# Optimization experiments

Hardware: AMD Instinct MI355X
Metric: run time of the kernel (lower is better)

## Reference

```python
import jax, jax.numpy as jnp
import numpy as np

N, E, D, H, G, C = 50000, 800000, 3, 128, 64, 10

def setup_inputs() -> dict:
    key = jax.random.key(0)
    ks = jax.random.split(key, 10)
    s = 0.1  # small init scale
    return {
        "pos": jax.random.normal(ks[0], (N, D), jnp.float32),
        "edge_index": jax.random.randint(ks[1], (2, E), 0, N, dtype=jnp.int64),
        "batch": jnp.sort(jax.random.randint(ks[2], (N,), 0, G, dtype=jnp.int64)),
        "W1": jax.random.normal(ks[3], (D, H), jnp.float32) * s,
        "b1": jnp.zeros((H,), jnp.float32),
        "W2": jax.random.normal(ks[4], (H, H), jnp.float32) * s,
        "b2": jnp.zeros((H,), jnp.float32),
        "W3": jax.random.normal(ks[5], (H, H), jnp.float32) * s,
        "b3": jnp.zeros((H,), jnp.float32),
        "Wl1": jax.random.normal(ks[6], (H, H // 2), jnp.float32) * s,
        "bl1": jnp.zeros((H // 2,), jnp.float32),
        "Wl2": jax.random.normal(ks[7], (H // 2, C), jnp.float32) * s,
        "bl2": jnp.zeros((C,), jnp.float32),
        "num_graphs": G,
    }

def reference(pos, edge_index, batch, W1, b1, W2, b2, W3, b3, Wl1, bl1, Wl2, bl2, num_graphs):
    n = pos.shape[0]
    loop = jnp.arange(n, dtype=edge_index.dtype)
    # GCN: add self-loops, symmetric normalization deg^-1/2 (A+I) deg^-1/2
    src = jnp.concatenate([edge_index[0], loop])
    dst = jnp.concatenate([edge_index[1], loop])
    deg = jax.ops.segment_sum(jnp.ones(src.shape, pos.dtype), dst, num_segments=n)
    dinv = jax.lax.rsqrt(jnp.maximum(deg, 1e-12))  # deg >= 1 due to self-loops
    norm = dinv[src] * dinv[dst]  # [E+N]

    def gcn(x, W, b):
        h = x @ W                               # [N,F] dense transform first (PyG order)
        msg = h[src] * norm[:, None]            # gather + normalize
        return jax.ops.segment_sum(msg, dst, num_segments=n) + b  # scatter-add

    x = jax.nn.relu(gcn(pos, W1, b1))   # dropout = identity (eval mode)
    x = jax.nn.relu(gcn(x, W2, b2))
    x = jax.nn.relu(gcn(x, W3, b3))
    # global_mean_pool over batch ids
    sums = jax.ops.segment_sum(x, batch, num_segments=num_graphs)
    cnt = jax.ops.segment_sum(jnp.ones((n,), x.dtype), batch, num_segments=num_graphs)
    g = sums / jnp.maximum(cnt, 1.0)[:, None]   # [G,H]
    h = jax.nn.relu(g @ Wl1 + bl1)
    return h @ Wl2 + bl2
```

## Files before the change

### kernel.cpp

```cpp
#include <hip/hip_runtime.h>

#define H 128
#define LSTRIDE 136
#define PSTR 132
typedef unsigned int uint32;
typedef unsigned short ushort16;
typedef __attribute__((ext_vector_type(8))) short bf16x8;
typedef __attribute__((ext_vector_type(4))) float f32x4;

static __device__ __forceinline__ ushort16 f2bf(float f){
  uint32 u = __float_as_uint(f);
  uint32 r = (u + 0x7fff + ((u >> 16) & 1)) >> 16;
  return (ushort16)r;
}
static __device__ __forceinline__ float bflo(uint32 u){ return __uint_as_float(u << 16); }
static __device__ __forceinline__ float bfhi(uint32 u){ return __uint_as_float(u & 0xffff0000u); }

__global__ __launch_bounds__(256) void k_setup(int* __restrict__ deg, float* __restrict__ gsum,
                                               const int* __restrict__ batch, int n, int G,
                                               int* __restrict__ gb, int SB,
                                               const float* __restrict__ W2, const float* __restrict__ W3,
                                               ushort16* __restrict__ wp2, ushort16* __restrict__ wp3){
  int b = blockIdx.x;
  if (b < SB){
    int i = b*256 + threadIdx.x;
    if (i < n) deg[i] = 0;
    if (i < G*H) gsum[i] = 0.f;
    if (i <= G){
      int lo = 0, hi = n;
      while (lo < hi){ int m = (lo + hi) >> 1; if (batch[m] < i) lo = m + 1; else hi = m; }
      gb[i] = lo;
    }
  } else {
    int gid = (b - SB)*256 + threadIdx.x;
    const float* W = (gid < 2048) ? W2 : W3;
    ushort16* wp   = (gid < 2048) ? wp2 : wp3;
    int tid = gid & 2047;
    int frag = tid >> 6, lane = tid & 63;
    int kt = frag >> 3, ct = frag & 7;
    int m = lane & 15, quad = lane >> 4;
    const float* wrow = &W[(kt*32 + quad*8)*H + ct*16 + m];
    ushort16 vals[8];
    #pragma unroll
    for (int j = 0; j < 8; j++) vals[j] = f2bf(wrow[j*H]);
    uint4 o;
    o.x = (uint32)vals[0] | ((uint32)vals[1] << 16);
    o.y = (uint32)vals[2] | ((uint32)vals[3] << 16);
    o.z = (uint32)vals[4] | ((uint32)vals[5] << 16);
    o.w = (uint32)vals[6] | ((uint32)vals[7] << 16);
    *(uint4*)&wp[(size_t)tid*8] = o;
  }
}

__global__ __launch_bounds__(256) void k_count_rank(const int* __restrict__ dst, int E,
                                                    int* __restrict__ deg, unsigned short* __restrict__ rank){
  int i = blockIdx.x*256 + threadIdx.x;
  if (i < E) rank[i] = (unsigned short)atomicAdd(&deg[dst[i]], 1);
}

__global__ __launch_bounds__(256) void k_scan1(const int* __restrict__ deg, int n,
      int* __restrict__ offsets, int* __restrict__ bsum, float* __restrict__ dinv){
  __shared__ int sh[256];
  int b = blockIdx.x, t = threadIdx.x;
  int base = b*1024 + t*4;
  bool i0 = base+0 < n, i1 = base+1 < n, i2 = base+2 < n, i3 = base+3 < n;
  int d0=0,d1=0,d2=0,d3=0;
  if (i3){ int4 v = *(const int4*)&deg[base]; d0=v.x; d1=v.y; d2=v.z; d3=v.w; }
  else {
    if (i0) d0 = deg[base+0];
    if (i1) d1 = deg[base+1];
    if (i2) d2 = deg[base+2];
  }
  int e0 = i0? d0+1:0, e1 = i1? d1+1:0, e2 = i2? d2+1:0, e3 = i3? d3+1:0;
  sh[t] = e0+e1+e2+e3;
  __syncthreads();
  for (int off=1; off<256; off<<=1){
    int v = sh[t];
    int add = (t>=off)? sh[t-off] : 0;
    __syncthreads();
    sh[t] = v+add;
    __syncthreads();
  }
  int o0 = (t==0)?0:sh[t-1];
  int o1 = o0+e0, o2 = o1+e1, o3 = o2+e2;
  if (i0){ offsets[base+0]=o0; dinv[base+0]=rsqrtf((float)(d0+1)); }
  if (i1){ offsets[base+1]=o1; dinv[base+1]=rsqrtf((float)(d1+1)); }
  if (i2){ offsets[base+2]=o2; dinv[base+2]=rsqrtf((float)(d2+1)); }
  if (i3){ offsets[base+3]=o3; dinv[base+3]=rsqrtf((float)(d3+1)); }
  if (t==255) bsum[b] = sh[255];
}

__global__ __launch_bounds__(256) void k_scan3b(int* __restrict__ offsets, int n,
                                                const int* __restrict__ bsum, int B){
  __shared__ int sh[2];
  int b = blockIdx.x, t = threadIdx.x;
  if (t < 64){
    int v   = (t < B)? bsum[t] : 0;
    int pre = (t < b)? v : 0;
    int tot = v;
    for (int o=1; o<64; o<<=1){ pre += __shfl_xor(pre,o); tot += __shfl_xor(tot,o); }
    if (t == 0){ sh[0] = pre; sh[1] = tot; }
  }
  __syncthreads();
  int add = sh[0];
  int base = b*1024 + t*4;
  if (base+3 < n){
    int4 v = *(int4*)&offsets[base];
    v.x+=add; v.y+=add; v.z+=add; v.w+=add;
    *(int4*)&offsets[base] = v;
  } else {
    #pragma unroll
    for (int k=0;k<4;k++){ int i=base+k; if (i<n) offsets[i]+=add; }
  }
  if (b == B-1 && t == 255) offsets[n] = sh[1];
}

__global__ __launch_bounds__(256) void k_fill2(const int* __restrict__ src, const int* __restrict__ dst,
            int E, int n, const int* __restrict__ offsets, const unsigned short* __restrict__ rank,
            unsigned short* __restrict__ csr_src){
  int i = blockIdx.x*256 + threadIdx.x;
  if (i < E){
    csr_src[offsets[dst[i]] + 1 + rank[i]] = (unsigned short)src[i];
  } else if (i < E + n){
    int j = i - E;
    csr_src[offsets[j]] = (unsigned short)j;
  }
}

__global__ __launch_bounds__(256) void k_prescale(const float* __restrict__ pos, const float* __restrict__ dinv,
                                                  float4* __restrict__ y0, int n){
  int i = blockIdx.x*256 + threadIdx.x;
  if (i < n){
    float d = dinv[i];
    y0[i] = make_float4(pos[3*i]*d, pos[3*i+1]*d, pos[3*i+2]*d, 0.f);
  }
}

__global__ __launch_bounds__(256) void k_layer1(const float4* __restrict__ y0, const int* __restrict__ offsets,
      const unsigned short* __restrict__ csr_src, const float* __restrict__ dinv,
      const float* __restrict__ W1, const float* __restrict__ b1,
      ushort16* __restrict__ y1, int n){
  int node = blockIdx.x*256 + threadIdx.x;
  if (node >= n) return;
  int lo = offsets[node], hi = offsets[node+1];
  float x=0.f, y=0.f, z=0.f;
  int e = lo;
  for (; e+2 <= hi; e += 2){
    int s0 = csr_src[e], s1 = csr_src[e+1];
    float4 v0 = y0[s0], v1 = y0[s1];
    x += v0.x + v1.x; y += v0.y + v1.y; z += v0.z + v1.z;
  }
  if (e < hi){ float4 v = y0[csr_src[e]]; x += v.x; y += v.y; z += v.z; }
  float dn = dinv[node];
  x *= dn; y *= dn; z *= dn;
  ushort16* rowp = &y1[(size_t)node*H];
  for (int c8 = 0; c8 < 16; c8++){
    float4 wa0 = *(const float4*)&W1[c8*8];
    float4 wa1 = *(const float4*)&W1[c8*8+4];
    float4 wb0 = *(const float4*)&W1[H + c8*8];
    float4 wb1 = *(const float4*)&W1[H + c8*8+4];
    float4 wc0 = *(const float4*)&W1[2*H + c8*8];
    float4 wc1 = *(const float4*)&W1[2*H + c8*8+4];
    float4 bb0 = *(const float4*)&b1[c8*8];
    float4 bb1 = *(const float4*)&b1[c8*8+4];
    float o0 = fmaxf(x*wa0.x + y*wb0.x + z*wc0.x + bb0.x, 0.f) * dn;
    float o1 = fmaxf(x*wa0.y + y*wb0.y + z*wc0.y + bb0.y, 0.f) * dn;
    float o2 = fmaxf(x*wa0.z + y*wb0.z + z*wc0.z + bb0.z, 0.f) * dn;
    float o3 = fmaxf(x*wa0.w + y*wb0.w + z*wc0.w + bb0.w, 0.f) * dn;
    float o4 = fmaxf(x*wa1.x + y*wb1.x + z*wc1.x + bb1.x, 0.f) * dn;
    float o5 = fmaxf(x*wa1.y + y*wb1.y + z*wc1.y + bb1.y, 0.f) * dn;
    float o6 = fmaxf(x*wa1.z + y*wb1.z + z*wc1.z + bb1.z, 0.f) * dn;
    float o7 = fmaxf(x*wa1.w + y*wb1.w + z*wc1.w + bb1.w, 0.f) * dn;
    uint4 o;
    o.x = (uint32)f2bf(o0) | ((uint32)f2bf(o1) << 16);
    o.y = (uint32)f2bf(o2) | ((uint32)f2bf(o3) << 16);
    o.z = (uint32)f2bf(o4) | ((uint32)f2bf(o5) << 16);
    o.w = (uint32)f2bf(o6) | ((uint32)f2bf(o7) << 16);
    *(uint4*)&rowp[c8*8] = o;
  }
}

template<int POOL>
__global__ __launch_bounds__(256) void k_aggdense(const ushort16* __restrict__ y, const int* __restrict__ offsets,
      const unsigned short* __restrict__ csr_src, const float* __restrict__ dinv, const ushort16* __restrict__ wp,
      const float* __restrict__ bias,
      ushort16* __restrict__ yout, const int* __restrict__ batch, float* __restrict__ gsum, int n){
  __shared__ unsigned short As[16*LSTRIDE];
  __shared__ float pool[POOL ? 16*PSTR : 1];
  __shared__ unsigned short outs[POOL ? 1 : 16*PSTR];
  __shared__ int sbatch[POOL ? 16 : 1];
  int tid = threadIdx.x;
  int node16 = blockIdx.x*16;
  int nl = tid >> 4;
  int node = node16 + nl;
  int f8 = (tid & 15) * 8;

  if (POOL && tid < 16) sbatch[tid] = (node16 + tid < n) ? batch[node16 + tid] : -1;

  float a0=0,a1=0,a2=0,a3=0,a4=0,a5=0,a6=0,a7=0;
  float dn = 0.f;
  #define ADDU(u) { a0+=bflo(u.x); a1+=bfhi(u.x); a2+=bflo(u.y); a3+=bfhi(u.y); \
                    a4+=bflo(u.z); a5+=bfhi(u.z); a6+=bflo(u.w); a7+=bfhi(u.w); }
  if (node < n){
    int lo = offsets[node], hi = offsets[node+1];
    int e = lo;
    for (; e+8 <= hi; e += 8){
      int s0=csr_src[e],   s1=csr_src[e+1], s2=csr_src[e+2], s3=csr_src[e+3];
      int s4=csr_src[e+4], s5=csr_src[e+5], s6=csr_src[e+6], s7=csr_src[e+7];
      uint4 u0 = *(const uint4*)&y[(size_t)s0*H + f8];
      uint4 u1 = *(const uint4*)&y[(size_t)s1*H + f8];
      uint4 u2 = *(const uint4*)&y[(size_t)s2*H + f8];
      uint4 u3 = *(const uint4*)&y[(size_t)s3*H + f8];
      uint4 u4 = *(const uint4*)&y[(size_t)s4*H + f8];
      uint4 u5 = *(const uint4*)&y[(size_t)s5*H + f8];
      uint4 u6 = *(const uint4*)&y[(size_t)s6*H + f8];
      uint4 u7 = *(const uint4*)&y[(size_t)s7*H + f8];
      ADDU(u0); ADDU(u1); ADDU(u2); ADDU(u3);
      ADDU(u4); ADDU(u5); ADDU(u6); ADDU(u7);
    }
    for (; e < hi; e++){
      int s = csr_src[e];
      uint4 u = *(const uint4*)&y[(size_t)s*H + f8];
      ADDU(u);
    }
    dn = dinv[node];
  }
  #undef ADDU
  uint4 o;
  o.x = (uint32)f2bf(a0*dn) | ((uint32)f2bf(a1*dn) << 16);
  o.y = (uint32)f2bf(a2*dn) | ((uint32)f2bf(a3*dn) << 16);
  o.z = (uint32)f2bf(a4*dn) | ((uint32)f2bf(a5*dn) << 16);
  o.w = (uint32)f2bf(a6*dn) | ((uint32)f2bf(a7*dn) << 16);
  *(uint4*)&As[nl*LSTRIDE + f8] = o;
  __syncthreads();

  int wave = tid >> 6;
  int lane = tid & 63;
  int m = lane & 15, quad = lane >> 4;
  f32x4 acc0 = {0.f,0.f,0.f,0.f}, acc1 = {0.f,0.f,0.f,0.f};
  int ct0 = wave*2, ct1 = wave*2 + 1;
  #pragma unroll
  for (int kt = 0; kt < 4; kt++){
    bf16x8 af = *(const bf16x8*)&As[m*LSTRIDE + kt*32 + quad*8];
    bf16x8 b0 = *(const bf16x8*)&wp[(size_t)((kt*8+ct0)*64 + lane)*8];
    bf16x8 b1 = *(const bf16x8*)&wp[(size_t)((kt*8+ct1)*64 + lane)*8];
    acc0 = __builtin_amdgcn_mfma_f32_16x16x32_bf16(af, b0, acc0, 0, 0, 0);
    acc1 = __builtin_amdgcn_mfma_f32_16x16x32_bf16(af, b1, acc1, 0, 0, 0);
  }
  #pragma unroll
  for (int j = 0; j < 2; j++){
    int ct = wave*2 + j;
    int col = ct*16 + m;
    float bv = bias[col];
    f32x4 ac = j ? acc1 : acc0;
    #pragma unroll
    for (int r = 0; r < 4; r++){
      int rl = quad*4 + r;
      int orow = node16 + rl;
      if (orow < n){
        float v = fmaxf(ac[r] + bv, 0.f);
        if (POOL) pool[rl*PSTR + col] = v;
        else      outs[rl*PSTR + col] = f2bf(v * dinv[orow]);
      }
    }
  }
  __syncthreads();
  if (POOL){
    int col = tid & 127;
    int half = tid >> 7;
    float run = 0.f; int gprev = -1;
    for (int r = half*8; r < half*8 + 8; r++){
      int g = sbatch[r];
      if (g < 0) break;
      if (g != gprev){
        if (gprev >= 0) atomicAdd(&gsum[gprev*H + col], run);
        run = 0.f; gprev = g;
      }
      run += pool[r*PSTR + col];
    }
    if (gprev >= 0) atomicAdd(&gsum[gprev*H + col], run);
  } else {
    int row = tid >> 4;
    int orow = node16 + row;
    if (orow < n){
      const unsigned short* sp = &outs[row*PSTR + f8];
      uint4 v;
      v.x = (uint32)sp[0] | ((uint32)sp[1] << 16);
      v.y = (uint32)sp[2] | ((uint32)sp[3] << 16);
      v.z = (uint32)sp[4] | ((uint32)sp[5] << 16);
      v.w = (uint32)sp[6] | ((uint32)sp[7] << 16);
      *(uint4*)&yout[(size_t)orow*H + f8] = v;
    }
  }
}

__global__ __launch_bounds__(64) void k_head(const float* __restrict__ gsum, const int* __restrict__ gb,
            const float* __restrict__ Wl1, const float* __restrict__ bl1,
            const float* __restrict__ Wl2, const float* __restrict__ bl2,
            float* __restrict__ out){
  int g = blockIdx.x;
  int t = threadIdx.x;
  __shared__ float gs[H];
  __shared__ float h1[64];
  float inv = 1.f / fmaxf((float)(gb[g+1] - gb[g]), 1.f);
  gs[t]      = gsum[g*H + t]      * inv;
  gs[64 + t] = gsum[g*H + 64 + t] * inv;
  __syncthreads();
  float acc = bl1[t];
  for (int k = 0; k < H; k++) acc += gs[k] * Wl1[k*64 + t];
  h1[t] = fmaxf(acc, 0.f);
  __syncthreads();
  if (t < 10){
    float o = bl2[t];
    for (int j = 0; j < 64; j++) o += h1[j] * Wl2[j*10 + t];
    out[g*10 + t] = o;
  }
}

extern "C" void kernel_launch(void* const* d_in, const int* in_sizes, int n_in,
                              void* d_out, int out_size, void* d_ws, size_t ws_size,
                              hipStream_t stream){
  const float* pos = (const float*)d_in[0];
  const int*  ei   = (const int*)d_in[1];
  const int*  batch= (const int*)d_in[2];
  const float* W1 = (const float*)d_in[3];
  const float* b1 = (const float*)d_in[4];
  const float* W2 = (const float*)d_in[5];
  const float* b2 = (const float*)d_in[6];
  const float* W3 = (const float*)d_in[7];
  const float* b3 = (const float*)d_in[8];
  const float* Wl1 = (const float*)d_in[9];
  const float* bl1 = (const float*)d_in[10];
  const float* Wl2 = (const float*)d_in[11];
  const float* bl2 = (const float*)d_in[12];
  float* out = (float*)d_out;

  int N = in_sizes[0] / 3;
  int E = in_sizes[1] / 2;
  int G = out_size / 10;
  int B = (N + 1023) / 1024;
  int SB = (N + 255) / 256;

  char* p = (char*)d_ws;
  auto carve = [&](size_t bytes)->char* { char* q = p; p += (bytes + 255) & ~(size_t)255; return q; };
  int*            deg     = (int*)     carve(sizeof(int)    * (size_t)N);
  int*            offsets = (int*)     carve(sizeof(int)    * (size_t)(N+1));
  float*          dinv    = (float*)   carve(sizeof(float)  * (size_t)N);
  int*            bsum    = (int*)     carve(sizeof(int)    * 256);
  int*            gb      = (int*)     carve(sizeof(int)    * (size_t)(G+1));
  float*          gsum    = (float*)   carve(sizeof(float)  * (size_t)G * H);
  unsigned short* csr_src = (unsigned short*)carve(sizeof(unsigned short) * (size_t)(E+N));
  unsigned short* rank    = (unsigned short*)carve(sizeof(unsigned short) * (size_t)E);
  float4*         y0      = (float4*)  carve(sizeof(float4) * (size_t)N);
  ushort16*       ybufA   = (ushort16*)carve(sizeof(ushort16) * (size_t)N * H);
  ushort16*       ybufB   = (ushort16*)carve(sizeof(ushort16) * (size_t)N * H);
  ushort16*       wp2     = (ushort16*)carve(sizeof(ushort16) * 16384);
  ushort16*       wp3     = (ushort16*)carve(sizeof(ushort16) * 16384);

  const int* src = ei;
  const int* dst = ei + E;

  hipLaunchKernelGGL(k_setup, dim3(SB + 16), dim3(256), 0, stream,
                     deg, gsum, batch, N, G, gb, SB, W2, W3, wp2, wp3);

  hipLaunchKernelGGL(k_count_rank, dim3((E+255)/256),   dim3(256), 0, stream, dst, E, deg, rank);
  hipLaunchKernelGGL(k_scan1,      dim3(B),             dim3(256), 0, stream, deg, N, offsets, bsum, dinv);
  hipLaunchKernelGGL(k_scan3b,     dim3(B),             dim3(256), 0, stream, offsets, N, bsum, B);
  hipLaunchKernelGGL(k_fill2,      dim3((E+N+255)/256), dim3(256), 0, stream, src, dst, E, N, offsets, rank, csr_src);

  hipLaunchKernelGGL(k_prescale, dim3((N+255)/256), dim3(256), 0, stream, pos, dinv, y0, N);
  hipLaunchKernelGGL(k_layer1,   dim3((N+255)/256), dim3(256), 0, stream, y0, offsets, csr_src, dinv, W1, b1, ybufA, N);

  hipLaunchKernelGGL(k_aggdense<0>, dim3((N+15)/16), dim3(256), 0, stream,
                     ybufA, offsets, csr_src, dinv, wp2, b2, ybufB, (const int*)nullptr, (float*)nullptr, N);

  hipLaunchKernelGGL(k_aggdense<1>, dim3((N+15)/16), dim3(256), 0, stream,
                     ybufB, offsets, csr_src, dinv, wp3, b3, (ushort16*)nullptr, batch, gsum, N);

  hipLaunchKernelGGL(k_head, dim3(G), dim3(64), 0, stream, gsum, gb, Wl1, bl1, Wl2, bl2, out);
}
```

Baseline: 254.7 us.

## Pad CSR rows to multiples of eight with dummy zero node, fuse prescale

Each CSR row is padded to a multiple of eight entries, with padding pointing at an extra all-zero row (index n) appended to y0 and both bf16 feature buffers. The gather loops can then read eight 16-bit indices with one 128-bit load and drop their remainder loops. The separate prescale kernel is folded into the scan kernel, removing one launch. In exchange the padding adds wasted gathers of the zero row (about 3.5 extra per node on average), and k_fill2 now writes the padding slots in a serial per-node loop.

```diff
diff --git a/kernel.cpp b/kernel.cpp
--- a/kernel.cpp
+++ b/kernel.cpp
@@ -20,12 +20,17 @@
                                                const int* __restrict__ batch, int n, int G,
                                                int* __restrict__ gb, int SB,
                                                const float* __restrict__ W2, const float* __restrict__ W3,
-                                               ushort16* __restrict__ wp2, ushort16* __restrict__ wp3){
+                                               ushort16* __restrict__ wp2, ushort16* __restrict__ wp3,
+                                               float4* __restrict__ y0,
+                                               unsigned short* __restrict__ ybA,
+                                               unsigned short* __restrict__ ybB){
   int b = blockIdx.x;
   if (b < SB){
     int i = b*256 + threadIdx.x;
     if (i < n) deg[i] = 0;
     if (i < G*H) gsum[i] = 0.f;
+    if (i < H){ ybA[(size_t)n*H + i] = 0; ybB[(size_t)n*H + i] = 0; }
+    if (i == 0) y0[n] = make_float4(0.f, 0.f, 0.f, 0.f);
     if (i <= G){
       int lo = 0, hi = n;
       while (lo < hi){ int m = (lo + hi) >> 1; if (batch[m] < i) lo = m + 1; else hi = m; }
@@ -59,7 +64,8 @@
 }
 
 __global__ __launch_bounds__(256) void k_scan1(const int* __restrict__ deg, int n,
-      int* __restrict__ offsets, int* __restrict__ bsum, float* __restrict__ dinv){
+      int* __restrict__ offsets, int* __restrict__ bsum, float* __restrict__ dinv,
+      const float* __restrict__ pos, float4* __restrict__ y0){
   __shared__ int sh[256];
   int b = blockIdx.x, t = threadIdx.x;
   int base = b*1024 + t*4;
@@ -71,7 +77,7 @@
     if (i1) d1 = deg[base+1];
     if (i2) d2 = deg[base+2];
   }
-  int e0 = i0? d0+1:0, e1 = i1? d1+1:0, e2 = i2? d2+1:0, e3 = i3? d3+1:0;
+  int e0 = i0? ((d0+8)&~7):0, e1 = i1? ((d1+8)&~7):0, e2 = i2? ((d2+8)&~7):0, e3 = i3? ((d3+8)&~7):0;
   sh[t] = e0+e1+e2+e3;
   __syncthreads();
   for (int off=1; off<256; off<<=1){
@@ -83,10 +89,25 @@
   }
   int o0 = (t==0)?0:sh[t-1];
   int o1 = o0+e0, o2 = o1+e1, o3 = o2+e2;
-  if (i0){ offsets[base+0]=o0; dinv[base+0]=rsqrtf((float)(d0+1)); }
-  if (i1){ offsets[base+1]=o1; dinv[base+1]=rsqrtf((float)(d1+1)); }
-  if (i2){ offsets[base+2]=o2; dinv[base+2]=rsqrtf((float)(d2+1)); }
-  if (i3){ offsets[base+3]=o3; dinv[base+3]=rsqrtf((float)(d3+1)); }
+  float dv0 = rsqrtf((float)(d0+1)), dv1 = rsqrtf((float)(d1+1));
+  float dv2 = rsqrtf((float)(d2+1)), dv3 = rsqrtf((float)(d3+1));
+  if (i0){ offsets[base+0]=o0; dinv[base+0]=dv0; }
+  if (i1){ offsets[base+1]=o1; dinv[base+1]=dv1; }
+  if (i2){ offsets[base+2]=o2; dinv[base+2]=dv2; }
+  if (i3){ offsets[base+3]=o3; dinv[base+3]=dv3; }
+  if (i3){
+    float4 p0 = *(const float4*)&pos[3*base];
+    float4 p1 = *(const float4*)&pos[3*base+4];
+    float4 p2 = *(const float4*)&pos[3*base+8];
+    y0[base+0] = make_float4(p0.x*dv0, p0.y*dv0, p0.z*dv0, 0.f);
+    y0[base+1] = make_float4(p0.w*dv1, p1.x*dv1, p1.y*dv1, 0.f);
+    y0[base+2] = make_float4(p1.z*dv2, p1.w*dv2, p2.x*dv2, 0.f);
+    y0[base+3] = make_float4(p2.y*dv3, p2.z*dv3, p2.w*dv3, 0.f);
+  } else {
+    if (i0) y0[base+0] = make_float4(pos[3*base+0]*dv0, pos[3*base+1]*dv0, pos[3*base+2]*dv0, 0.f);
+    if (i1) y0[base+1] = make_float4(pos[3*base+3]*dv1, pos[3*base+4]*dv1, pos[3*base+5]*dv1, 0.f);
+    if (i2) y0[base+2] = make_float4(pos[3*base+6]*dv2, pos[3*base+7]*dv2, pos[3*base+8]*dv2, 0.f);
+  }
   if (t==255) bsum[b] = sh[255];
 }
 
@@ -116,23 +137,17 @@
 }
 
 __global__ __launch_bounds__(256) void k_fill2(const int* __restrict__ src, const int* __restrict__ dst,
-            int E, int n, const int* __restrict__ offsets, const unsigned short* __restrict__ rank,
-            unsigned short* __restrict__ csr_src){
+            int E, int n, const int* __restrict__ offsets, const int* __restrict__ deg,
+            const unsigned short* __restrict__ rank, unsigned short* __restrict__ csr_src){
   int i = blockIdx.x*256 + threadIdx.x;
   if (i < E){
     csr_src[offsets[dst[i]] + 1 + rank[i]] = (unsigned short)src[i];
   } else if (i < E + n){
     int j = i - E;
-    csr_src[offsets[j]] = (unsigned short)j;
-  }
-}
-
-__global__ __launch_bounds__(256) void k_prescale(const float* __restrict__ pos, const float* __restrict__ dinv,
-                                                  float4* __restrict__ y0, int n){
-  int i = blockIdx.x*256 + threadIdx.x;
-  if (i < n){
-    float d = dinv[i];
-    y0[i] = make_float4(pos[3*i]*d, pos[3*i+1]*d, pos[3*i+2]*d, 0.f);
+    int o = offsets[j];
+    csr_src[o] = (unsigned short)j;
+    int end = offsets[j+1];
+    for (int s2 = o + 1 + deg[j]; s2 < end; s2++) csr_src[s2] = (unsigned short)n;
   }
 }
 
@@ -144,13 +159,18 @@
   if (node >= n) return;
   int lo = offsets[node], hi = offsets[node+1];
   float x=0.f, y=0.f, z=0.f;
-  int e = lo;
-  for (; e+2 <= hi; e += 2){
-    int s0 = csr_src[e], s1 = csr_src[e+1];
-    float4 v0 = y0[s0], v1 = y0[s1];
-    x += v0.x + v1.x; y += v0.y + v1.y; z += v0.z + v1.z;
-  }
-  if (e < hi){ float4 v = y0[csr_src[e]]; x += v.x; y += v.y; z += v.z; }
+  for (int e = lo; e < hi; e += 8){
+    uint4 iv = *(const uint4*)&csr_src[e];
+    int s0 = iv.x & 0xffff, s1 = iv.x >> 16;
+    int s2 = iv.y & 0xffff, s3 = iv.y >> 16;
+    int s4 = iv.z & 0xffff, s5 = iv.z >> 16;
+    int s6 = iv.w & 0xffff, s7 = iv.w >> 16;
+    float4 v0 = y0[s0], v1 = y0[s1], v2 = y0[s2], v3 = y0[s3];
+    float4 v4 = y0[s4], v5 = y0[s5], v6 = y0[s6], v7 = y0[s7];
+    x += ((v0.x+v1.x)+(v2.x+v3.x)) + ((v4.x+v5.x)+(v6.x+v7.x));
+    y += ((v0.y+v1.y)+(v2.y+v3.y)) + ((v4.y+v5.y)+(v6.y+v7.y));
+    z += ((v0.z+v1.z)+(v2.z+v3.z)) + ((v4.z+v5.z)+(v6.z+v7.z));
+  }
   float dn = dinv[node];
   x *= dn; y *= dn; z *= dn;
   ushort16* rowp = &y1[(size_t)node*H];
@@ -203,10 +223,13 @@
                     a4+=bflo(u.z); a5+=bfhi(u.z); a6+=bflo(u.w); a7+=bfhi(u.w); }
   if (node < n){
     int lo = offsets[node], hi = offsets[node+1];
-    int e = lo;
-    for (; e+8 <= hi; e += 8){
-      int s0=csr_src[e],   s1=csr_src[e+1], s2=csr_src[e+2], s3=csr_src[e+3];
-      int s4=csr_src[e+4], s5=csr_src[e+5], s6=csr_src[e+6], s7=csr_src[e+7];
+    dn = dinv[node];
+    for (int e = lo; e < hi; e += 8){
+      uint4 iv = *(const uint4*)&csr_src[e];
+      int s0 = iv.x & 0xffff, s1 = iv.x >> 16;
+      int s2 = iv.y & 0xffff, s3 = iv.y >> 16;
+      int s4 = iv.z & 0xffff, s5 = iv.z >> 16;
+      int s6 = iv.w & 0xffff, s7 = iv.w >> 16;
       uint4 u0 = *(const uint4*)&y[(size_t)s0*H + f8];
       uint4 u1 = *(const uint4*)&y[(size_t)s1*H + f8];
       uint4 u2 = *(const uint4*)&y[(size_t)s2*H + f8];
@@ -218,12 +241,6 @@
       ADDU(u0); ADDU(u1); ADDU(u2); ADDU(u3);
       ADDU(u4); ADDU(u5); ADDU(u6); ADDU(u7);
     }
-    for (; e < hi; e++){
-      int s = csr_src[e];
-      uint4 u = *(const uint4*)&y[(size_t)s*H + f8];
-      ADDU(u);
-    }
-    dn = dinv[node];
   }
   #undef ADDU
   uint4 o;
@@ -349,11 +366,11 @@
   int*            bsum    = (int*)     carve(sizeof(int)    * 256);
   int*            gb      = (int*)     carve(sizeof(int)    * (size_t)(G+1));
   float*          gsum    = (float*)   carve(sizeof(float)  * (size_t)G * H);
-  unsigned short* csr_src = (unsigned short*)carve(sizeof(unsigned short) * (size_t)(E+N));
+  unsigned short* csr_src = (unsigned short*)carve(sizeof(unsigned short) * ((size_t)E + 8*(size_t)N));
   unsigned short* rank    = (unsigned short*)carve(sizeof(unsigned short) * (size_t)E);
-  float4*         y0      = (float4*)  carve(sizeof(float4) * (size_t)N);
-  ushort16*       ybufA   = (ushort16*)carve(sizeof(ushort16) * (size_t)N * H);
-  ushort16*       ybufB   = (ushort16*)carve(sizeof(ushort16) * (size_t)N * H);
+  float4*         y0      = (float4*)  carve(sizeof(float4) * (size_t)(N+1));
+  ushort16*       ybufA   = (ushort16*)carve(sizeof(ushort16) * (size_t)(N+1) * H);
+  ushort16*       ybufB   = (ushort16*)carve(sizeof(ushort16) * (size_t)(N+1) * H);
   ushort16*       wp2     = (ushort16*)carve(sizeof(ushort16) * 16384);
   ushort16*       wp3     = (ushort16*)carve(sizeof(ushort16) * 16384);
 
@@ -361,14 +378,14 @@
   const int* dst = ei + E;
 
   hipLaunchKernelGGL(k_setup, dim3(SB + 16), dim3(256), 0, stream,
-                     deg, gsum, batch, N, G, gb, SB, W2, W3, wp2, wp3);
+                     deg, gsum, batch, N, G, gb, SB, W2, W3, wp2, wp3,
+                     y0, (unsigned short*)ybufA, (unsigned short*)ybufB);
 
   hipLaunchKernelGGL(k_count_rank, dim3((E+255)/256),   dim3(256), 0, stream, dst, E, deg, rank);
-  hipLaunchKernelGGL(k_scan1,      dim3(B),             dim3(256), 0, stream, deg, N, offsets, bsum, dinv);
+  hipLaunchKernelGGL(k_scan1,      dim3(B),             dim3(256), 0, stream, deg, N, offsets, bsum, dinv, pos, y0);
   hipLaunchKernelGGL(k_scan3b,     dim3(B),             dim3(256), 0, stream, offsets, N, bsum, B);
-  hipLaunchKernelGGL(k_fill2,      dim3((E+N+255)/256), dim3(256), 0, stream, src, dst, E, N, offsets, rank, csr_src);
-
-  hipLaunchKernelGGL(k_prescale, dim3((N+255)/256), dim3(256), 0, stream, pos, dinv, y0, N);
+  hipLaunchKernelGGL(k_fill2,      dim3((E+N+255)/256), dim3(256), 0, stream, src, dst, E, N, offsets, deg, rank, csr_src);
+
   hipLaunchKernelGGL(k_layer1,   dim3((N+255)/256), dim3(256), 0, stream, y0, offsets, csr_src, dinv, W1, b1, ybufA, N);
 
   hipLaunchKernelGGL(k_aggdense<0>, dim3((N+15)/16), dim3(256), 0, stream,
```

Result: faster. 239.5 us (-6.0%).
